# Optimization experiments

Measured on AMD Instinct MI355X. Metric: run time of the kernel, lower is better.

Reference implementation:

```python
import jax, jax.numpy as jnp
import numpy as np

WINDOW = 128
SOFTCLAMP = 50.0


def setup_inputs() -> dict:
    key = jax.random.key(0)
    ks = jax.random.split(key, 5)
    b, h, n, d = 1, 16, 16384, 32
    nw, w = n // WINDOW, WINDOW
    q = jax.random.normal(ks[0], (b, h, n, d), dtype=jnp.float32)
    k = jax.random.normal(ks[1], (b, h, n, d), dtype=jnp.float32)
    v = jax.random.normal(ks[2], (b, h, n, d), dtype=jnp.float32)
    mask = jnp.ones((b, n), dtype=bool)
    # windowed attention bias: [b, nw, w, 2w]
    attn_bias = jax.random.normal(ks[3], (b, nw, w, 2 * w), dtype=jnp.float32)
    # memory key/value slots: [2, h, m, d]
    memory_kv = jax.random.normal(ks[4], (2, h, 4, d), dtype=jnp.float32)
    return {"q": q, "k": k, "v": v, "mask": mask,
            "attn_bias": attn_bias, "memory_kv": memory_kv}


def _local_attn(q, k, v, mask, attn_bias, memory_kv):
    b, h, n, d = q.shape
    w = WINDOW
    pad = (w - n % w) % w
    if pad > 0:
        q = jnp.pad(q, ((0, 0), (0, 0), (0, pad), (0, 0)))
        k = jnp.pad(k, ((0, 0), (0, 0), (0, pad), (0, 0)))
        v = jnp.pad(v, ((0, 0), (0, 0), (0, pad), (0, 0)))
        mask = jnp.pad(mask, ((0, 0), (0, pad)), constant_values=False)
    np_ = q.shape[-2]
    nw = np_ // w
    scale = d ** -0.5
    qw = q.reshape(b, h, nw, w, d) * scale        # (b,h,nw,w,d)
    kw = k.reshape(b, h, nw, w, d)
    vw = v.reshape(b, h, nw, w, d)
    mw = mask.reshape(b, nw, w)
    # prepend a zero window, then concat previous + current window -> 2w keys
    kp = jnp.pad(kw, ((0, 0), (0, 0), (1, 0), (0, 0), (0, 0)))
    vp = jnp.pad(vw, ((0, 0), (0, 0), (1, 0), (0, 0), (0, 0)))
    mp = jnp.pad(mw, ((0, 0), (1, 0), (0, 0)), constant_values=False)
    k2 = jnp.concatenate([kp[:, :, :-1], kp[:, :, 1:]], axis=-2)  # (b,h,nw,2w,d)
    v2 = jnp.concatenate([vp[:, :, :-1], vp[:, :, 1:]], axis=-2)
    m2 = jnp.concatenate([mp[:, :-1], mp[:, 1:]], axis=-1)        # (b,nw,2w)
    # memory key/values, broadcast over batch and windows
    mk, mv = memory_kv[0], memory_kv[1]                            # (h,m,d)
    nm = mk.shape[-2]
    mk_b = jnp.broadcast_to(mk[None, :, None], (b, h, nw, nm, d))
    mv_b = jnp.broadcast_to(mv[None, :, None], (b, h, nw, nm, d))
    k2 = jnp.concatenate([mk_b, k2], axis=-2)                      # (b,h,nw,nm+2w,d)
    v2 = jnp.concatenate([mv_b, v2], axis=-2)
    bias = jnp.pad(attn_bias, ((0, 0), (0, 0), (0, 0), (nm, 0)))   # (b,nw,w,nm+2w)
    m2 = jnp.pad(m2, ((0, 0), (0, 0), (nm, 0)), constant_values=True)
    sim = jnp.einsum('bhnid,bhnjd->bhnij', qw, k2)                 # (b,h,nw,w,nm+2w)
    sim = sim + bias[:, None]
    sim = SOFTCLAMP * jnp.tanh(sim / SOFTCLAMP)
    neg = -jnp.finfo(sim.dtype).max
    sim = jnp.where(m2[:, None, :, None, :], sim, neg)
    attn = jax.nn.softmax(sim, axis=-1)
    out = jnp.einsum('bhnij,bhnjd->bhnid', attn, v2)
    out = out.reshape(b, h, np_, d)[..., :n, :]
    return out


def reference(q, k, v, mask, attn_bias, memory_kv):
    return _local_attn(q, k, v, mask, attn_bias, memory_kv)
```

## Files before the change

kernel.cpp:

```cpp
#include <hip/hip_runtime.h>
#include <hip/hip_bf16.h>


#define H    16
#define NTOK 16384
#define D    32
#define W    128
#define NM   4

#define NROW      416
#define VT_OFF    26624
#define VT_STRIDE 848
#define LDS_BYTES (26624 + 32 * 848)

#define BT_BYTES  ((size_t)512 * 9 * 512 * 4)

typedef float f32x4  __attribute__((ext_vector_type(4)));
typedef float f32x16 __attribute__((ext_vector_type(16)));
typedef short bf16x8 __attribute__((ext_vector_type(8)));

__device__ __forceinline__ unsigned cvtpk(float lo, float hi) {
    unsigned r;
    asm("v_cvt_pk_bf16_f32 %0, %1, %2" : "=v"(r) : "v"(lo), "v"(hi));
    return r;
}
__device__ __forceinline__ float exp2_fast(float x) {
#if __has_builtin(__builtin_amdgcn_exp2f)
    return __builtin_amdgcn_exp2f(x);
#else
    return __expf(x * 0.6931471805599453f);
#endif
}

__global__ __launch_bounds__(256) void bias_pack_bf16(
    const float* __restrict__ bias, unsigned* __restrict__ bt)
{
    __shared__ float tile[32][260];
    const int b  = blockIdx.x;
    const int t  = threadIdx.x;
    const int wi = b >> 2;

    const float* src = bias + ((size_t)b) * 32 * 256;
#pragma unroll
    for (int e = 0; e < 8; ++e) {
        const int idx = t + e * 256;
        const int row = idx >> 6;
        const int c4  = (idx & 63) * 4;
        *(f32x4*)&tile[row][c4] = *(const f32x4*)(src + row * 256 + c4);
    }
    __syncthreads();

    const int lane = t >> 2;
    const int jg   = t & 3;
    const int l31  = lane & 31;
    const int h    = lane >> 5;
    const float NINF = -__builtin_inff();
    unsigned* dst = bt + ((size_t)b * 9) * 512 + lane * 8 + jg * 2;
#pragma unroll
    for (int c = 0; c < 9; ++c) {
        const int key0 = 32 * c + 8 * jg + 4 * h;
        float vv[4];
#pragma unroll
        for (int i = 0; i < 4; ++i) {
            const int key = key0 + i;
            const int col = key - 16;
            const bool mk = (key >= 4 && key < 16) ||
                            (wi == 0 && key >= 16 && key < 144) ||
                            (key >= 272);
            const float bv = (col >= 0 && col < 256) ? tile[l31][col] : 0.f;
            vv[i] = mk ? NINF : bv;
        }
        uint2 wd;
        wd.x = cvtpk(vv[0], vv[1]);
        wd.y = cvtpk(vv[2], vv[3]);
        *(uint2*)(dst + (size_t)c * 512) = wd;
    }
}

__global__ __launch_bounds__(512, 4) void attn_local_mfma15(
    const float* __restrict__ q, const float* __restrict__ k,
    const float* __restrict__ v, const unsigned* __restrict__ bt,
    const float* __restrict__ mkv, float* __restrict__ out)
{
    __shared__ __align__(16) char smem[LDS_BYTES];
    char* Kb = smem;
    char* Vb = smem + VT_OFF;

    const int blk0 = blockIdx.x;
    const int blk  = (blk0 & 7) * 128 + (blk0 >> 3);

    const int hh   = blk & (H - 1);
    const int wi0  = (blk >> 4) * 2;
    const int tid  = threadIdx.x;
    const int lane = tid & 63;
    const int wid  = tid >> 6;
    const int ww   = wid >> 2;
    const int qt   = wid & 3;
    const int l31  = lane & 31;
    const int h    = lane >> 5;
    const int wi   = wi0 + ww;

    const float* qp = q + ((size_t)hh * NTOK + wi * W + qt * 32 + l31) * D;
    const f32x4 q0 = *(const f32x4*)(qp + 8 * h);
    const f32x4 q1 = *(const f32x4*)(qp + 8 * h + 4);
    const f32x4 q2 = *(const f32x4*)(qp + 16 + 8 * h);
    const f32x4 q3 = *(const f32x4*)(qp + 16 + 8 * h + 4);

    float4 ka[7], va[7];
    int    rowA[7], dgA[7];
#pragma unroll
    for (int u = 0; u < 7; ++u) {
        int idx = tid + u * 512;
        if (idx >= NROW * 8) idx = tid;
        const int rr = idx >> 3;
        const int dg = idx & 7;
        rowA[u] = rr; dgA[u] = dg;
        const int  t     = (wi0 - 1) * W + rr - 16;
        const bool ismem = rr < NM;
        const bool valid = ismem || (rr >= 16 && rr < 400 && t >= 0);
        const int  tc    = (valid && !ismem) ? t : 0;
        const float* kp = ismem ? (mkv + ((size_t)hh * NM + rr) * D + dg * 4)
                                : (k + ((size_t)hh * NTOK + tc) * D + dg * 4);
        const float* vp = ismem ? (mkv + ((size_t)(H + hh) * NM + rr) * D + dg * 4)
                                : (v + ((size_t)hh * NTOK + tc) * D + dg * 4);
        ka[u] = *(const float4*)kp;
        va[u] = *(const float4*)vp;
    }
#pragma unroll
    for (int u = 0; u < 7; ++u) {
        const int rr = rowA[u], dg = dgA[u];
        uint2 kd;
        kd.x = cvtpk(ka[u].x, ka[u].y);
        kd.y = cvtpk(ka[u].z, ka[u].w);
        const int slot = (dg >> 1) ^ (rr & 3);
        *(uint2*)(Kb + rr * 64 + slot * 16 + (dg & 1) * 8) = kd;
        const float vvA[4] = {va[u].x, va[u].y, va[u].z, va[u].w};
#pragma unroll
        for (int c2 = 0; c2 < 4; ++c2) {
            const int d = dg * 4 + c2;
            *(unsigned short*)(Vb + d * VT_STRIDE + rr * 2) =
                (unsigned short)cvtpk(vvA[c2], vvA[c2]);
        }
    }

    const float SC = 0.17677669529663687f;
    union UB { bf16x8 hx; unsigned u[4]; };
    UB qf1, qf2;
    qf1.u[0] = cvtpk(q0.x * SC, q0.y * SC); qf1.u[1] = cvtpk(q0.z * SC, q0.w * SC);
    qf1.u[2] = cvtpk(q1.x * SC, q1.y * SC); qf1.u[3] = cvtpk(q1.z * SC, q1.w * SC);
    qf2.u[0] = cvtpk(q2.x * SC, q2.y * SC); qf2.u[1] = cvtpk(q2.z * SC, q2.w * SC);
    qf2.u[2] = cvtpk(q3.x * SC, q3.y * SC); qf2.u[3] = cvtpk(q3.z * SC, q3.w * SC);

    __syncthreads();

    const unsigned* btp = bt + ((size_t)(wi * 4 + qt) * 9) * 512 + lane * 8;
    const float L2E = 1.4426950408889634f;
    const float B50 = -72.13475204444817f;

    f32x16 O;
#pragma unroll
    for (int j = 0; j < 16; ++j) O[j] = 0.f;
    float ls0 = 0.f, ls1 = 0.f, ls2 = 0.f, ls3 = 0.f;

    uint4 bw0 = *(const uint4*)(btp);
    uint4 bw1 = *(const uint4*)(btp + 4);

#pragma unroll 1
    for (int c = 0; c < 9; ++c) {
        const int cn = (c < 8) ? c + 1 : 8;
        const uint4 nb0 = *(const uint4*)(btp + (size_t)cn * 512);
        const uint4 nb1 = *(const uint4*)(btp + (size_t)cn * 512 + 4);

        const unsigned uw[8] = {bw0.x, bw0.y, bw0.z, bw0.w,
                                bw1.x, bw1.y, bw1.z, bw1.w};
        f32x16 cc;
#pragma unroll
        for (int w = 0; w < 8; ++w) {
            cc[2 * w]     = __uint_as_float(uw[w] << 16);
            cc[2 * w + 1] = __uint_as_float(uw[w] & 0xFFFF0000u);
        }

        const int kk  = 32 * c + l31;
        const int row = kk + ((kk < 16) ? 0 : ww * W);
        const char* krow = Kb + row * 64;
        const bf16x8 kf1 = *(const bf16x8*)(krow + (((h)     ^ (row & 3)) << 4));
        const bf16x8 kf2 = *(const bf16x8*)(krow + (((2 + h) ^ (row & 3)) << 4));

        const int kv0 = 32 * c + 8 * h;
        const int cs0 = kv0 + ((kv0 < 16) ? 0 : ww * W);
        const int kv1 = 32 * c + 16 + 8 * h;
        const int cs1 = kv1 + ((kv1 < 16) ? 0 : ww * W);
        const bf16x8 vf0 = *(const bf16x8*)(Vb + l31 * VT_STRIDE + cs0 * 2);
        const bf16x8 vf1 = *(const bf16x8*)(Vb + l31 * VT_STRIDE + cs1 * 2);

        f32x16 S = __builtin_amdgcn_mfma_f32_32x32x16_bf16(kf1, qf1.hx, cc, 0, 0, 0);
        S = __builtin_amdgcn_mfma_f32_32x32x16_bf16(kf2, qf2.hx, S, 0, 0, 0);

        float p[16];
#pragma unroll
        for (int j = 0; j < 16; ++j) {
            const float s  = S[j];
            const float u2 = s * s;
            const float t1 = __builtin_fmaf(u2, 2.1333333e-8f, -1.3333333e-4f);
            const float w2 = __builtin_fmaf(u2, t1, 1.0f);
            p[j] = exp2_fast(__builtin_fmaf(s * L2E, w2, B50));
        }
        ls0 += (p[0] + p[4]) + (p[8] + p[12]);
        ls1 += (p[1] + p[5]) + (p[9] + p[13]);
        ls2 += (p[2] + p[6]) + (p[10] + p[14]);
        ls3 += (p[3] + p[7]) + (p[11] + p[15]);

        unsigned Dw[8];
#pragma unroll
        for (int i = 0; i < 8; ++i) Dw[i] = cvtpk(p[2 * i], p[2 * i + 1]);

        UB A1, A2;
        {
            unsigned a0 = Dw[0], b0 = Dw[2];
            asm volatile("v_permlane32_swap_b32 %0, %1" : "+v"(a0), "+v"(b0));
            unsigned a1 = Dw[1], b1 = Dw[3];
            asm volatile("v_permlane32_swap_b32 %0, %1" : "+v"(a1), "+v"(b1));
            A1.u[0] = a0; A1.u[1] = a1; A1.u[2] = b0; A1.u[3] = b1;
        }
        {
            unsigned a0 = Dw[4], b0 = Dw[6];
            asm volatile("v_permlane32_swap_b32 %0, %1" : "+v"(a0), "+v"(b0));
            unsigned a1 = Dw[5], b1 = Dw[7];
            asm volatile("v_permlane32_swap_b32 %0, %1" : "+v"(a1), "+v"(b1));
            A2.u[0] = a0; A2.u[1] = a1; A2.u[2] = b0; A2.u[3] = b1;
        }

        O = __builtin_amdgcn_mfma_f32_32x32x16_bf16(A1.hx, vf0, O, 0, 0, 0);
        O = __builtin_amdgcn_mfma_f32_32x32x16_bf16(A2.hx, vf1, O, 0, 0, 0);

        bw0 = nb0; bw1 = nb1;
    }

    float lsum = (ls0 + ls1) + (ls2 + ls3);
    lsum += __shfl_xor(lsum, 32, 64);
    const float rdn = __builtin_amdgcn_rcpf(lsum);

    const size_t obase = ((size_t)hh * NTOK + wi * W + qt * 32) * D + l31;
#pragma unroll
    for (int j = 0; j < 16; ++j) {
        const int qr = (j & 3) + 8 * (j >> 2) + 4 * h;
        const float rd = __shfl(rdn, qr, 64);
        out[obase + (size_t)qr * D] = O[j] * rd;
    }
}

__global__ __launch_bounds__(512, 4) void attn_local_mfma10(
    const float* __restrict__ q, const float* __restrict__ k,
    const float* __restrict__ v, const float* __restrict__ bias,
    const float* __restrict__ mkv, float* __restrict__ out)
{
    __shared__ __align__(16) char smem[LDS_BYTES];
    char* Kb = smem;
    char* Vbf = smem + VT_OFF;

    const int blk  = blockIdx.x;
    const int hh   = blk & (H - 1);
    const int wi0  = (blk >> 4) * 2;
    const int tid  = threadIdx.x;
    const int lane = tid & 63;
    const int wid  = tid >> 6;
    const int ww   = wid >> 2;
    const int qt   = wid & 3;
    const int l31  = lane & 31;
    const int h    = lane >> 5;

    const float* qp = q + ((size_t)hh * NTOK + (wi0 + ww) * W + qt * 32 + l31) * D;
    const f32x4 q0 = *(const f32x4*)(qp + 8 * h);
    const f32x4 q1 = *(const f32x4*)(qp + 8 * h + 4);
    const f32x4 q2 = *(const f32x4*)(qp + 16 + 8 * h);
    const f32x4 q3 = *(const f32x4*)(qp + 16 + 8 * h + 4);

    float4 ka[7], va[7];
    float  mm[7];
    int    rowA[7], dgA[7];
#pragma unroll
    for (int u = 0; u < 7; ++u) {
        int idx = tid + u * 512;
        if (idx >= NROW * 8) idx = tid;
        const int rr = idx >> 3;
        const int dg = idx & 7;
        rowA[u] = rr; dgA[u] = dg;
        const int  t     = (wi0 - 1) * W + rr - 16;
        const bool ismem = rr < NM;
        const bool valid = ismem || (rr >= 16 && rr < 400 && t >= 0);
        const int  tc    = (valid && !ismem) ? t : 0;
        const float* kp = ismem ? (mkv + ((size_t)hh * NM + rr) * D + dg * 4)
                                : (k + ((size_t)hh * NTOK + tc) * D + dg * 4);
        const float* vp = ismem ? (mkv + ((size_t)(H + hh) * NM + rr) * D + dg * 4)
                                : (v + ((size_t)hh * NTOK + tc) * D + dg * 4);
        ka[u] = *(const float4*)kp;
        va[u] = *(const float4*)vp;
        mm[u] = valid ? 1.f : 0.f;
    }
#pragma unroll
    for (int u = 0; u < 7; ++u) {
        const int rr = rowA[u], dg = dgA[u];
        const float m = mm[u];
        uint2 kd;
        kd.x = cvtpk(ka[u].x * m, ka[u].y * m);
        kd.y = cvtpk(ka[u].z * m, ka[u].w * m);
        const int slot = (dg >> 1) ^ (rr & 3);
        *(uint2*)(Kb + rr * 64 + slot * 16 + (dg & 1) * 8) = kd;
        const float vvA[4] = {va[u].x * m, va[u].y * m, va[u].z * m, va[u].w * m};
#pragma unroll
        for (int c2 = 0; c2 < 4; ++c2) {
            const int d = dg * 4 + c2;
            *(unsigned short*)(Vbf + d * VT_STRIDE + rr * 2) =
                (unsigned short)cvtpk(vvA[c2], vvA[c2]);
        }
    }

    const float SC = 0.17677669529663687f;
    union UB { bf16x8 hx; unsigned u[4]; };
    UB qf1, qf2;
    qf1.u[0] = cvtpk(q0.x * SC, q0.y * SC); qf1.u[1] = cvtpk(q0.z * SC, q0.w * SC);
    qf1.u[2] = cvtpk(q1.x * SC, q1.y * SC); qf1.u[3] = cvtpk(q1.z * SC, q1.w * SC);
    qf2.u[0] = cvtpk(q2.x * SC, q2.y * SC); qf2.u[1] = cvtpk(q2.z * SC, q2.w * SC);
    qf2.u[2] = cvtpk(q3.x * SC, q3.y * SC); qf2.u[3] = cvtpk(q3.z * SC, q3.w * SC);

    __syncthreads();

    const float* brow = bias + ((size_t)((wi0 + ww) * W + qt * 32 + l31)) * (2 * W);
    const bool skip8 = (wi0 + ww) == 0;
    const float L2E = 1.4426950408889634f;
    const float B50 = -72.13475204444817f;

    f32x16 O;
#pragma unroll
    for (int j = 0; j < 16; ++j) O[j] = 0.f;
    float ls0 = 0.f, ls1 = 0.f, ls2 = 0.f, ls3 = 0.f;

#pragma unroll 1
    for (int c = 0; c < 9; ++c) {
        const int kk  = 32 * c + l31;
        const int row = kk + ((kk < 16) ? 0 : ww * W);
        const char* krow = Kb + row * 64;
        const bf16x8 kf1 = *(const bf16x8*)(krow + (((h)     ^ (row & 3)) << 4));
        const bf16x8 kf2 = *(const bf16x8*)(krow + (((2 + h) ^ (row & 3)) << 4));

        const int kv0 = 32 * c + 8 * h;
        const int cs0 = kv0 + ((kv0 < 16) ? 0 : ww * W);
        const int kv1 = 32 * c + 16 + 8 * h;
        const int cs1 = kv1 + ((kv1 < 16) ? 0 : ww * W);
        const bf16x8 vf0 = *(const bf16x8*)(Vbf + l31 * VT_STRIDE + cs0 * 2);
        const bf16x8 vf1 = *(const bf16x8*)(Vbf + l31 * VT_STRIDE + cs1 * 2);

        f32x16 cc;
#pragma unroll
        for (int g2 = 0; g2 < 4; ++g2) {
            f32x4 bb = {0.f, 0.f, 0.f, 0.f};
            if (!(c == 0 && g2 < 2)) {
                int colg = 32 * c - 16 + 8 * g2 + 4 * h;
                colg = (colg > 252) ? 252 : colg;
                bb = *(const f32x4*)(brow + colg);
            }
            cc[4 * g2 + 0] = bb[0]; cc[4 * g2 + 1] = bb[1];
            cc[4 * g2 + 2] = bb[2]; cc[4 * g2 + 3] = bb[3];
        }

        f32x16 S = __builtin_amdgcn_mfma_f32_32x32x16_bf16(kf1, qf1.hx, cc, 0, 0, 0);
        S = __builtin_amdgcn_mfma_f32_32x32x16_bf16(kf2, qf2.hx, S, 0, 0, 0);

        float mres[4];
#pragma unroll
        for (int g2 = 0; g2 < 4; ++g2) {
            const int base = 32 * c + 8 * g2 + 4 * h;
            const bool mk = (base >= 4 && base < 16) ||
                            (skip8 && base >= 16 && base < 144) ||
                            (base >= 272);
            mres[g2] = mk ? -1e30f : B50;
        }

        float p[16];
#pragma unroll
        for (int j = 0; j < 16; ++j) {
            const float s  = S[j];
            const float u2 = s * s;
            const float t1 = __builtin_fmaf(u2, 2.1333333e-8f, -1.3333333e-4f);
            const float w2 = __builtin_fmaf(u2, t1, 1.0f);
            p[j] = exp2_fast(__builtin_fmaf(s * L2E, w2, mres[j >> 2]));
        }
        ls0 += (p[0] + p[4]) + (p[8] + p[12]);
        ls1 += (p[1] + p[5]) + (p[9] + p[13]);
        ls2 += (p[2] + p[6]) + (p[10] + p[14]);
        ls3 += (p[3] + p[7]) + (p[11] + p[15]);

        unsigned Dw[8];
#pragma unroll
        for (int i = 0; i < 8; ++i) Dw[i] = cvtpk(p[2 * i], p[2 * i + 1]);

        UB A1, A2;
        {
            unsigned a0 = Dw[0], b0 = Dw[2];
            asm volatile("v_permlane32_swap_b32 %0, %1" : "+v"(a0), "+v"(b0));
            unsigned a1 = Dw[1], b1 = Dw[3];
            asm volatile("v_permlane32_swap_b32 %0, %1" : "+v"(a1), "+v"(b1));
            A1.u[0] = a0; A1.u[1] = a1; A1.u[2] = b0; A1.u[3] = b1;
        }
        {
            unsigned a0 = Dw[4], b0 = Dw[6];
            asm volatile("v_permlane32_swap_b32 %0, %1" : "+v"(a0), "+v"(b0));
            unsigned a1 = Dw[5], b1 = Dw[7];
            asm volatile("v_permlane32_swap_b32 %0, %1" : "+v"(a1), "+v"(b1));
            A2.u[0] = a0; A2.u[1] = a1; A2.u[2] = b0; A2.u[3] = b1;
        }

        O = __builtin_amdgcn_mfma_f32_32x32x16_bf16(A1.hx, vf0, O, 0, 0, 0);
        O = __builtin_amdgcn_mfma_f32_32x32x16_bf16(A2.hx, vf1, O, 0, 0, 0);
    }

    float lsum = (ls0 + ls1) + (ls2 + ls3);
    lsum += __shfl_xor(lsum, 32, 64);
    const float rdn = __builtin_amdgcn_rcpf(lsum);

    const size_t obase = ((size_t)hh * NTOK + (wi0 + ww) * W + qt * 32) * D + l31;
#pragma unroll
    for (int j = 0; j < 16; ++j) {
        const int qr = (j & 3) + 8 * (j >> 2) + 4 * h;
        const float rd = __shfl(rdn, qr, 64);
        out[obase + (size_t)qr * D] = O[j] * rd;
    }
}

extern "C" void kernel_launch(void* const* d_in, const int* in_sizes, int n_in,
                              void* d_out, int out_size, void* d_ws, size_t ws_size,
                              hipStream_t stream)
{
    const float* q    = (const float*)d_in[0];
    const float* k    = (const float*)d_in[1];
    const float* v    = (const float*)d_in[2];
    const float* bias = (const float*)d_in[4];
    const float* mkv  = (const float*)d_in[5];
    float* out = (float*)d_out;

    if (ws_size >= BT_BYTES) {
        unsigned* bt = (unsigned*)d_ws;
        hipLaunchKernelGGL(bias_pack_bf16, dim3(512), dim3(256), 0, stream,
                           bias, bt);
        hipLaunchKernelGGL(attn_local_mfma15, dim3(64 * H), dim3(512), 0, stream,
                           q, k, v, bt, mkv, out);
    } else {
        hipLaunchKernelGGL(attn_local_mfma10, dim3(64 * H), dim3(512), 0, stream,
                           q, k, v, bias, mkv, out);
    }
}
```

Before: 47.28 us.

## Process one window per block instead of two to shrink LDS and raise parallelism

Each workgroup now handles a single 128-token window with 4 waves (256 threads) instead of two windows with 8 waves, and the grid doubles. The staged K/V tile shrinks from 416 rows to 272 rows, cutting LDS per block and simplifying the row-offset math in the inner loop. The cost is that neighbouring windows no longer share their overlapping previous-window K/V loads within a block, so global K/V traffic per output rises.

Measured after the change: 47.52 us. Within noise of the previous version (+0.5%).

```diff
diff --git a/kernel.cpp b/kernel.cpp
--- a/kernel.cpp
+++ b/kernel.cpp
@@ -8,10 +8,9 @@
 #define W    128
 #define NM   4
 
-#define NROW      416
-#define VT_OFF    26624
-#define VT_STRIDE 848
-#define LDS_BYTES (26624 + 32 * 848)
+#define KROWS     272
+#define VT_STRIDE 560
+#define LDS_BYTES (KROWS * 64 + 32 * VT_STRIDE)
 
 #define BT_BYTES  ((size_t)512 * 9 * 512 * 4)
 
@@ -77,28 +76,25 @@
     }
 }
 
-__global__ __launch_bounds__(512, 4) void attn_local_mfma15(
+__global__ __launch_bounds__(256, 4) void attn_local_mfma16(
     const float* __restrict__ q, const float* __restrict__ k,
     const float* __restrict__ v, const unsigned* __restrict__ bt,
     const float* __restrict__ mkv, float* __restrict__ out)
 {
     __shared__ __align__(16) char smem[LDS_BYTES];
     char* Kb = smem;
-    char* Vb = smem + VT_OFF;
+    char* Vb = smem + KROWS * 64;
 
     const int blk0 = blockIdx.x;
-    const int blk  = (blk0 & 7) * 128 + (blk0 >> 3);
+    const int blk  = (blk0 & 7) * 256 + (blk0 >> 3);
 
     const int hh   = blk & (H - 1);
-    const int wi0  = (blk >> 4) * 2;
+    const int wi   = blk >> 4;
     const int tid  = threadIdx.x;
     const int lane = tid & 63;
-    const int wid  = tid >> 6;
-    const int ww   = wid >> 2;
-    const int qt   = wid & 3;
+    const int qt   = tid >> 6;
     const int l31  = lane & 31;
     const int h    = lane >> 5;
-    const int wi   = wi0 + ww;
 
     const float* qp = q + ((size_t)hh * NTOK + wi * W + qt * 32 + l31) * D;
     const f32x4 q0 = *(const f32x4*)(qp + 8 * h);
@@ -106,40 +102,46 @@
     const f32x4 q2 = *(const f32x4*)(qp + 16 + 8 * h);
     const f32x4 q3 = *(const f32x4*)(qp + 16 + 8 * h + 4);
 
-    float4 ka[7], va[7];
-    int    rowA[7], dgA[7];
-#pragma unroll
-    for (int u = 0; u < 7; ++u) {
-        int idx = tid + u * 512;
-        if (idx >= NROW * 8) idx = tid;
-        const int rr = idx >> 3;
-        const int dg = idx & 7;
-        rowA[u] = rr; dgA[u] = dg;
-        const int  t     = (wi0 - 1) * W + rr - 16;
-        const bool ismem = rr < NM;
-        const bool valid = ismem || (rr >= 16 && rr < 400 && t >= 0);
-        const int  tc    = (valid && !ismem) ? t : 0;
-        const float* kp = ismem ? (mkv + ((size_t)hh * NM + rr) * D + dg * 4)
-                                : (k + ((size_t)hh * NTOK + tc) * D + dg * 4);
-        const float* vp = ismem ? (mkv + ((size_t)(H + hh) * NM + rr) * D + dg * 4)
-                                : (v + ((size_t)hh * NTOK + tc) * D + dg * 4);
-        ka[u] = *(const float4*)kp;
-        va[u] = *(const float4*)vp;
-    }
-#pragma unroll
-    for (int u = 0; u < 7; ++u) {
-        const int rr = rowA[u], dg = dgA[u];
-        uint2 kd;
-        kd.x = cvtpk(ka[u].x, ka[u].y);
-        kd.y = cvtpk(ka[u].z, ka[u].w);
-        const int slot = (dg >> 1) ^ (rr & 3);
-        *(uint2*)(Kb + rr * 64 + slot * 16 + (dg & 1) * 8) = kd;
-        const float vvA[4] = {va[u].x, va[u].y, va[u].z, va[u].w};
-#pragma unroll
-        for (int c2 = 0; c2 < 4; ++c2) {
-            const int d = dg * 4 + c2;
-            *(unsigned short*)(Vb + d * VT_STRIDE + rr * 2) =
-                (unsigned short)cvtpk(vvA[c2], vvA[c2]);
+#pragma unroll
+    for (int it = 0; it < 3; ++it) {
+        float4 ka[3], va[3];
+        int rows[3], dgs[3];
+#pragma unroll
+        for (int u = 0; u < 3; ++u) {
+            const int idx = tid + (it * 3 + u) * 256;
+            const int rr = idx >> 3;
+            const int dg = idx & 7;
+            rows[u] = rr; dgs[u] = dg;
+            const int  t     = (wi - 1) * W + rr - 16;
+            const bool ismem = rr < NM;
+            const bool valid = rr >= 16 && rr < 272 && t >= 0;
+            const int  tc    = valid ? t : 0;
+            const float* kp = ismem ? (mkv + ((size_t)hh * NM + rr) * D + dg * 4)
+                                    : (k + ((size_t)hh * NTOK + tc) * D + dg * 4);
+            const float* vp = ismem ? (mkv + ((size_t)(H + hh) * NM + rr) * D + dg * 4)
+                                    : (v + ((size_t)hh * NTOK + tc) * D + dg * 4);
+            ka[u] = *(const float4*)kp;
+            va[u] = *(const float4*)vp;
+        }
+#pragma unroll
+        for (int u = 0; u < 3; ++u) {
+            const int rr = rows[u], dg = dgs[u];
+            if (rr < KROWS) {
+                uint2 kd;
+                kd.x = cvtpk(ka[u].x, ka[u].y);
+                kd.y = cvtpk(ka[u].z, ka[u].w);
+                const int slot = (dg >> 1) ^ (rr & 3);
+                *(uint2*)(Kb + rr * 64 + slot * 16 + (dg & 1) * 8) = kd;
+            }
+            if (rr < 272) {
+                const float vvA[4] = {va[u].x, va[u].y, va[u].z, va[u].w};
+#pragma unroll
+                for (int c2 = 0; c2 < 4; ++c2) {
+                    const int d = dg * 4 + c2;
+                    *(unsigned short*)(Vb + d * VT_STRIDE + rr * 2) =
+                        (unsigned short)cvtpk(vvA[c2], vvA[c2]);
+                }
+            }
         }
     }
 
@@ -181,15 +183,13 @@
         }
 
         const int kk  = 32 * c + l31;
-        const int row = kk + ((kk < 16) ? 0 : ww * W);
+        const int row = (kk < KROWS) ? kk : (KROWS - 1);
         const char* krow = Kb + row * 64;
         const bf16x8 kf1 = *(const bf16x8*)(krow + (((h)     ^ (row & 3)) << 4));
         const bf16x8 kf2 = *(const bf16x8*)(krow + (((2 + h) ^ (row & 3)) << 4));
 
-        const int kv0 = 32 * c + 8 * h;
-        const int cs0 = kv0 + ((kv0 < 16) ? 0 : ww * W);
-        const int kv1 = 32 * c + 16 + 8 * h;
-        const int cs1 = kv1 + ((kv1 < 16) ? 0 : ww * W);
+        const int cs0 = 32 * c + 8 * h;
+        const int cs1 = (c < 8) ? (32 * c + 16 + 8 * h) : 256;
         const bf16x8 vf0 = *(const bf16x8*)(Vb + l31 * VT_STRIDE + cs0 * 2);
         const bf16x8 vf1 = *(const bf16x8*)(Vb + l31 * VT_STRIDE + cs1 * 2);
 
@@ -249,69 +249,70 @@
     }
 }
 
-__global__ __launch_bounds__(512, 4) void attn_local_mfma10(
+__global__ __launch_bounds__(256, 4) void attn_local_fb(
     const float* __restrict__ q, const float* __restrict__ k,
     const float* __restrict__ v, const float* __restrict__ bias,
     const float* __restrict__ mkv, float* __restrict__ out)
 {
     __shared__ __align__(16) char smem[LDS_BYTES];
     char* Kb = smem;
-    char* Vbf = smem + VT_OFF;
+    char* Vb = smem + KROWS * 64;
 
     const int blk  = blockIdx.x;
     const int hh   = blk & (H - 1);
-    const int wi0  = (blk >> 4) * 2;
+    const int wi   = blk >> 4;
     const int tid  = threadIdx.x;
     const int lane = tid & 63;
-    const int wid  = tid >> 6;
-    const int ww   = wid >> 2;
-    const int qt   = wid & 3;
+    const int qt   = tid >> 6;
     const int l31  = lane & 31;
     const int h    = lane >> 5;
 
-    const float* qp = q + ((size_t)hh * NTOK + (wi0 + ww) * W + qt * 32 + l31) * D;
+    const float* qp = q + ((size_t)hh * NTOK + wi * W + qt * 32 + l31) * D;
     const f32x4 q0 = *(const f32x4*)(qp + 8 * h);
     const f32x4 q1 = *(const f32x4*)(qp + 8 * h + 4);
     const f32x4 q2 = *(const f32x4*)(qp + 16 + 8 * h);
     const f32x4 q3 = *(const f32x4*)(qp + 16 + 8 * h + 4);
 
-    float4 ka[7], va[7];
-    float  mm[7];
-    int    rowA[7], dgA[7];
-#pragma unroll
-    for (int u = 0; u < 7; ++u) {
-        int idx = tid + u * 512;
-        if (idx >= NROW * 8) idx = tid;
-        const int rr = idx >> 3;
-        const int dg = idx & 7;
-        rowA[u] = rr; dgA[u] = dg;
-        const int  t     = (wi0 - 1) * W + rr - 16;
-        const bool ismem = rr < NM;
-        const bool valid = ismem || (rr >= 16 && rr < 400 && t >= 0);
-        const int  tc    = (valid && !ismem) ? t : 0;
-        const float* kp = ismem ? (mkv + ((size_t)hh * NM + rr) * D + dg * 4)
-                                : (k + ((size_t)hh * NTOK + tc) * D + dg * 4);
-        const float* vp = ismem ? (mkv + ((size_t)(H + hh) * NM + rr) * D + dg * 4)
-                                : (v + ((size_t)hh * NTOK + tc) * D + dg * 4);
-        ka[u] = *(const float4*)kp;
-        va[u] = *(const float4*)vp;
-        mm[u] = valid ? 1.f : 0.f;
-    }
-#pragma unroll
-    for (int u = 0; u < 7; ++u) {
-        const int rr = rowA[u], dg = dgA[u];
-        const float m = mm[u];
-        uint2 kd;
-        kd.x = cvtpk(ka[u].x * m, ka[u].y * m);
-        kd.y = cvtpk(ka[u].z * m, ka[u].w * m);
-        const int slot = (dg >> 1) ^ (rr & 3);
-        *(uint2*)(Kb + rr * 64 + slot * 16 + (dg & 1) * 8) = kd;
-        const float vvA[4] = {va[u].x * m, va[u].y * m, va[u].z * m, va[u].w * m};
-#pragma unroll
-        for (int c2 = 0; c2 < 4; ++c2) {
-            const int d = dg * 4 + c2;
-            *(unsigned short*)(Vbf + d * VT_STRIDE + rr * 2) =
-                (unsigned short)cvtpk(vvA[c2], vvA[c2]);
+#pragma unroll
+    for (int it = 0; it < 3; ++it) {
+        float4 ka[3], va[3];
+        int rows[3], dgs[3];
+#pragma unroll
+        for (int u = 0; u < 3; ++u) {
+            const int idx = tid + (it * 3 + u) * 256;
+            const int rr = idx >> 3;
+            const int dg = idx & 7;
+            rows[u] = rr; dgs[u] = dg;
+            const int  t     = (wi - 1) * W + rr - 16;
+            const bool ismem = rr < NM;
+            const bool valid = rr >= 16 && rr < 272 && t >= 0;
+            const int  tc    = valid ? t : 0;
+            const float* kp = ismem ? (mkv + ((size_t)hh * NM + rr) * D + dg * 4)
+                                    : (k + ((size_t)hh * NTOK + tc) * D + dg * 4);
+            const float* vp = ismem ? (mkv + ((size_t)(H + hh) * NM + rr) * D + dg * 4)
+                                    : (v + ((size_t)hh * NTOK + tc) * D + dg * 4);
+            ka[u] = *(const float4*)kp;
+            va[u] = *(const float4*)vp;
+        }
+#pragma unroll
+        for (int u = 0; u < 3; ++u) {
+            const int rr = rows[u], dg = dgs[u];
+            if (rr < KROWS) {
+                uint2 kd;
+                kd.x = cvtpk(ka[u].x, ka[u].y);
+                kd.y = cvtpk(ka[u].z, ka[u].w);
+                const int slot = (dg >> 1) ^ (rr & 3);
+                *(uint2*)(Kb + rr * 64 + slot * 16 + (dg & 1) * 8) = kd;
+            }
+            if (rr < 272) {
+                const float vvA[4] = {va[u].x, va[u].y, va[u].z, va[u].w};
+#pragma unroll
+                for (int c2 = 0; c2 < 4; ++c2) {
+                    const int d = dg * 4 + c2;
+                    *(unsigned short*)(Vb + d * VT_STRIDE + rr * 2) =
+                        (unsigned short)cvtpk(vvA[c2], vvA[c2]);
+                }
+            }
         }
     }
 
@@ -325,8 +326,8 @@
 
     __syncthreads();
 
-    const float* brow = bias + ((size_t)((wi0 + ww) * W + qt * 32 + l31)) * (2 * W);
-    const bool skip8 = (wi0 + ww) == 0;
+    const float* brow = bias + ((size_t)(wi * W + qt * 32 + l31)) * (2 * W);
+    const bool skip8 = (wi == 0);
     const float L2E = 1.4426950408889634f;
     const float B50 = -72.13475204444817f;
 
@@ -338,17 +339,15 @@
 #pragma unroll 1
     for (int c = 0; c < 9; ++c) {
         const int kk  = 32 * c + l31;
-        const int row = kk + ((kk < 16) ? 0 : ww * W);
+        const int row = (kk < KROWS) ? kk : (KROWS - 1);
         const char* krow = Kb + row * 64;
         const bf16x8 kf1 = *(const bf16x8*)(krow + (((h)     ^ (row & 3)) << 4));
         const bf16x8 kf2 = *(const bf16x8*)(krow + (((2 + h) ^ (row & 3)) << 4));
 
-        const int kv0 = 32 * c + 8 * h;
-        const int cs0 = kv0 + ((kv0 < 16) ? 0 : ww * W);
-        const int kv1 = 32 * c + 16 + 8 * h;
-        const int cs1 = kv1 + ((kv1 < 16) ? 0 : ww * W);
-        const bf16x8 vf0 = *(const bf16x8*)(Vbf + l31 * VT_STRIDE + cs0 * 2);
-        const bf16x8 vf1 = *(const bf16x8*)(Vbf + l31 * VT_STRIDE + cs1 * 2);
+        const int cs0 = 32 * c + 8 * h;
+        const int cs1 = (c < 8) ? (32 * c + 16 + 8 * h) : 256;
+        const bf16x8 vf0 = *(const bf16x8*)(Vb + l31 * VT_STRIDE + cs0 * 2);
+        const bf16x8 vf1 = *(const bf16x8*)(Vb + l31 * VT_STRIDE + cs1 * 2);
 
         f32x16 cc;
 #pragma unroll
@@ -418,7 +417,7 @@
     lsum += __shfl_xor(lsum, 32, 64);
     const float rdn = __builtin_amdgcn_rcpf(lsum);
 
-    const size_t obase = ((size_t)hh * NTOK + (wi0 + ww) * W + qt * 32) * D + l31;
+    const size_t obase = ((size_t)hh * NTOK + wi * W + qt * 32) * D + l31;
 #pragma unroll
     for (int j = 0; j < 16; ++j) {
         const int qr = (j & 3) + 8 * (j >> 2) + 4 * h;
@@ -442,10 +441,10 @@
         unsigned* bt = (unsigned*)d_ws;
         hipLaunchKernelGGL(bias_pack_bf16, dim3(512), dim3(256), 0, stream,
                            bias, bt);
-        hipLaunchKernelGGL(attn_local_mfma15, dim3(64 * H), dim3(512), 0, stream,
+        hipLaunchKernelGGL(attn_local_mfma16, dim3(128 * H), dim3(256), 0, stream,
                            q, k, v, bt, mkv, out);
     } else {
-        hipLaunchKernelGGL(attn_local_mfma10, dim3(64 * H), dim3(512), 0, stream,
+        hipLaunchKernelGGL(attn_local_fb, dim3(128 * H), dim3(256), 0, stream,
                            q, k, v, bias, mkv, out);
     }
 }
```
